# Optimization experiments

Measured on AMD Instinct MI355X. Metric: run time of the kernel, lower is better.

The kernel has to match this reference:

```python
import jax, jax.numpy as jnp
import numpy as np

N, DEG, F, H, OUT = 50000, 16, 128, 128, 64


def _lstm_aggr(neigh, w_ih, w_hh, b_ih, b_hh):
    # neigh: [N, D, F] fixed-degree neighbor features; run LSTM over D steps,
    # return final hidden state [N, H] (PyG SAGEConv 'lstm' aggregation).
    n, d, f = neigh.shape
    h_dim = w_hh.shape[1]

    def step(carry, xt):
        h, c = carry
        gates = xt @ w_ih.T + b_ih + h @ w_hh.T + b_hh  # [N, 4H]
        i, fg, g, o = jnp.split(gates, 4, axis=-1)      # torch gate order i,f,g,o
        i = jax.nn.sigmoid(i)
        fg = jax.nn.sigmoid(fg)
        g = jnp.tanh(g)
        o = jax.nn.sigmoid(o)
        c = fg * c + i * g
        h = o * jnp.tanh(c)
        return (h, c), None

    h0 = jnp.zeros((n, h_dim), neigh.dtype)
    (h, _), _ = jax.lax.scan(step, (h0, h0), jnp.swapaxes(neigh, 0, 1))
    return h


def _sage_lstm(x, src, w_ih, w_hh, b_ih, b_hh, wl, bl, wr):
    # SAGEConv: out = lin_l(lstm_aggr(x[neighbors])) + lin_r(x)
    neigh = x[src]                                   # [N, D, F] gather
    aggr = _lstm_aggr(neigh, w_ih, w_hh, b_ih, b_hh)  # [N, H]
    return aggr @ wl.T + bl + x @ wr.T


def setup_inputs() -> dict:
    key = jax.random.key(0)
    ks = jax.random.split(key, 16)
    x = jax.random.normal(ks[0], (N, F), dtype=jnp.float32)
    # fixed-degree graph: dst = arange(N) each repeated DEG times (sorted, as
    # PyG lstm aggregation requires), src random -> edge_index [2, N*DEG]
    src = jax.random.randint(ks[1], (N * DEG,), 0, N, dtype=jnp.int64)
    dst = jnp.repeat(jnp.arange(N, dtype=jnp.int64), DEG)
    edge_index = jnp.stack([src, dst])
    s = 1.0 / np.sqrt(H)
    def u(k, shape):
        return jax.random.uniform(k, shape, jnp.float32, -s, s)
    params = {
        # layer 1 (input F -> hidden H)
        "w_ih1": u(ks[2], (4 * H, F)), "w_hh1": u(ks[3], (4 * H, H)),
        "b_ih1": u(ks[4], (4 * H,)), "b_hh1": u(ks[5], (4 * H,)),
        "lin_l1_w": u(ks[6], (H, H)), "lin_l1_b": u(ks[6], (H,)),
        "lin_r1_w": u(ks[7], (H, F)),
        # layer 2 (H -> H)
        "w_ih2": u(ks[8], (4 * H, H)), "w_hh2": u(ks[9], (4 * H, H)),
        "b_ih2": u(ks[10], (4 * H,)), "b_hh2": u(ks[11], (4 * H,)),
        "lin_l2_w": u(ks[12], (H, H)), "lin_l2_b": u(ks[12], (H,)),
        "lin_r2_w": u(ks[13], (H, H)),
        # output head
        "lin_w": u(ks[14], (OUT, H)), "lin_b": u(ks[15], (OUT,)),
    }
    return {"x": x, "edge_index": edge_index, **params}


def reference(x, edge_index,
              w_ih1, w_hh1, b_ih1, b_hh1, lin_l1_w, lin_l1_b, lin_r1_w,
              w_ih2, w_hh2, b_ih2, b_hh2, lin_l2_w, lin_l2_b, lin_r2_w,
              lin_w, lin_b):
    n = x.shape[0]
    deg = edge_index.shape[1] // n
    src = edge_index[0].reshape(n, deg)  # fixed-degree neighbor matrix
    h = _sage_lstm(x, src, w_ih1, w_hh1, b_ih1, b_hh1, lin_l1_w, lin_l1_b, lin_r1_w)
    h = jax.nn.relu(h)
    h = _sage_lstm(h, src, w_ih2, w_hh2, b_ih2, b_hh2, lin_l2_w, lin_l2_b, lin_r2_w)
    h = jax.nn.relu(h)
    return h @ lin_w.T + lin_b
```

## Files before the change

### kernel.cpp

```cpp
#include <hip/hip_runtime.h>
#include <stdint.h>

#define NN 50000
#define DEG 16
#define MT 32
#define NBLK ((NN + MT - 1) / MT)
#define LOG2E 1.4426950408889634f

typedef short bf16x8 __attribute__((ext_vector_type(8)));
typedef float f32x4 __attribute__((ext_vector_type(4)));
typedef unsigned short u16;
typedef unsigned int u32;

static __device__ __forceinline__ u16 f2bf(float f) {
  union { float f; u32 u; } v; v.f = f;
  u32 u = v.u + 0x7FFFu + ((v.u >> 16) & 1u);
  return (u16)(u >> 16);
}
static __device__ __forceinline__ float rcp_(float x) {
  return __builtin_amdgcn_rcpf(x);
}
static __device__ __forceinline__ float ex2_(float x) {
  return __builtin_amdgcn_exp2f(x);
}
static __device__ __forceinline__ void gload_lds16(const void* g, void* l) {
  __builtin_amdgcn_global_load_lds(
      (const __attribute__((address_space(1))) void*)g,
      (__attribute__((address_space(3))) void*)l, 16, 0, 0);
}

__global__ void k_prep(const float* __restrict__ x, u16* __restrict__ xb,
                       const float* __restrict__ wih1, const float* __restrict__ whh1, u16* __restrict__ wpk1,
                       const float* __restrict__ wih2, const float* __restrict__ whh2, u16* __restrict__ wpk2,
                       const float* __restrict__ lr1, const float* __restrict__ ll1, u16* __restrict__ epk1,
                       const float* __restrict__ lr2, const float* __restrict__ ll2, u16* __restrict__ epk2,
                       const float* __restrict__ linw, u16* __restrict__ hpk,
                       const float* __restrict__ bi1, const float* __restrict__ bh1, float* __restrict__ bs1,
                       const float* __restrict__ bi2, const float* __restrict__ bh2, float* __restrict__ bs2) {
  int b = blockIdx.x;
  if (b < 128) {
    const float* wih = (b < 64) ? wih1 : wih2;
    const float* whh = (b < 64) ? whh1 : whh2;
    u16* wpk = (b < 64) ? wpk1 : wpk2;
    int t = (b & 63) * 256 + threadIdx.x;
    int lane = t & 63, kt = (t >> 6) & 7, g = (t >> 9) & 3, w = (t >> 11) & 7;
    int col = g * 128 + w * 16 + (lane & 15);
    int k0 = kt * 32 + (lane >> 4) * 8;
    float sc = (g == 2) ? 2.f * LOG2E : LOG2E;
#pragma unroll
    for (int j = 0; j < 8; ++j) {
      int k = k0 + j;
      float v = (k < 128) ? wih[col * 128 + k] : whh[col * 128 + k - 128];
      wpk[t * 8 + j] = f2bf(sc * v);
    }
  } else if (b < 160) {
    const float* lrw = (b < 144) ? lr1 : lr2;
    const float* llw = (b < 144) ? ll1 : ll2;
    u16* epk = (b < 144) ? epk1 : epk2;
    int t = ((b - 128) & 15) * 256 + threadIdx.x;
    int lane = t & 63, kt = (t >> 6) & 7, w = (t >> 9) & 7;
    int col = w * 16 + (lane & 15);
    int k0 = kt * 32 + (lane >> 4) * 8;
#pragma unroll
    for (int j = 0; j < 8; ++j) {
      int k = k0 + j;
      epk[t * 8 + j] = f2bf(k < 128 ? lrw[col * 128 + k] : llw[col * 128 + k - 128]);
    }
  } else if (b < 164) {
    int t = (b - 160) * 256 + threadIdx.x;
    int lane = t & 63, kt = (t >> 6) & 3, w = (t >> 8) & 3;
    int col = w * 16 + (lane & 15);
    int k0 = kt * 32 + (lane >> 4) * 8;
#pragma unroll
    for (int j = 0; j < 8; ++j) hpk[t * 8 + j] = f2bf(linw[col * 128 + k0 + j]);
  } else if (b < 168) {
    int t = (b - 164) * 256 + threadIdx.x;
    if (t < 1024) {
      int i = t & 511;
      float sc = ((i >> 7) == 2) ? 2.f * LOG2E : LOG2E;
      if (t < 512) bs1[i] = sc * (bi1[i] + bh1[i]);
      else bs2[i] = sc * (bi2[i] + bh2[i]);
    }
  } else {
    int i = (b - 168) * 256 + threadIdx.x;
    int stride = (gridDim.x - 168) * 256;
    for (; i < NN * 128 / 4; i += stride) {
      float4 v = ((const float4*)x)[i];
      ushort4 o;
      o.x = f2bf(v.x); o.y = f2bf(v.y); o.z = f2bf(v.z); o.w = f2bf(v.w);
      ((ushort4*)xb)[i] = o;
    }
  }
}


#define GATHER(DCODE, PDST)                                                   \
  do {                                                                        \
    int idx_;                                                                 \
    if ((DCODE) < DEG) idx_ = IDX[grow * DEG + (DCODE)];                      \
    else idx_ = (node0 + grow < NN) ? node0 + grow : NN - 1;                  \
    const char* gsw_ = (const char*)(xin + (size_t)idx_ * 128) +              \
                       ((lr * 16) ^ ((grow & 15) << 4));                      \
    gload_lds16(gsw_, (PDST) + (w * 4) * 128);                                \
  } while (0)

#define GATE_XPART(ACC, PSRC)                                                 \
  do {                                                                        \
    _Pragma("unroll") for (int mt = 0; mt < 2; ++mt)                          \
        _Pragma("unroll") for (int g = 0; g < 4; ++g)                         \
            ACC[mt][g] = (f32x4){gb[g], gb[g], gb[g], gb[g]};                 \
    _Pragma("unroll") for (int kt = 0; kt < 4; ++kt) {                        \
      bf16x8 af0 = *(const bf16x8*)((const char*)(PSRC) + lr * 256 +          \
                                    ((kt * 64 + lh * 16) ^ ((lr & 15) << 4))); \
      bf16x8 af1 = *(const bf16x8*)((const char*)(PSRC) + (16 + lr) * 256 +   \
                                    ((kt * 64 + lh * 16) ^ ((lr & 15) << 4))); \
      _Pragma("unroll") for (int g = 0; g < 4; ++g) {                         \
        ACC[0][g] = __builtin_amdgcn_mfma_f32_16x16x32_bf16(af0, wreg[g][kt], ACC[0][g], 0, 0, 0); \
        ACC[1][g] = __builtin_amdgcn_mfma_f32_16x16x32_bf16(af1, wreg[g][kt], ACC[1][g], 0, 0, 0); \
      }                                                                       \
    }                                                                         \
  } while (0)

#define GATE_HPART(ACC, PSRC)                                                 \
  do {                                                                        \
    _Pragma("unroll") for (int kt = 0; kt < 4; ++kt) {                        \
      bf16x8 af0 = *(const bf16x8*)((const char*)(PSRC) + lr * 256 +          \
                                    ((kt * 64 + lh * 16) ^ ((lr & 15) << 4))); \
      bf16x8 af1 = *(const bf16x8*)((const char*)(PSRC) + (16 + lr) * 256 +   \
                                    ((kt * 64 + lh * 16) ^ ((lr & 15) << 4))); \
      _Pragma("unroll") for (int g = 0; g < 4; ++g) {                         \
        ACC[0][g] = __builtin_amdgcn_mfma_f32_16x16x32_bf16(af0, wreg[g][4 + kt], ACC[0][g], 0, 0, 0); \
        ACC[1][g] = __builtin_amdgcn_mfma_f32_16x16x32_bf16(af1, wreg[g][4 + kt], ACC[1][g], 0, 0, 0); \
      }                                                                       \
    }                                                                         \
  } while (0)

#define GATE_EW(ACC, AHDST)                                                   \
  do {                                                                        \
    _Pragma("unroll") for (int mt = 0; mt < 2; ++mt)                          \
        _Pragma("unroll") for (int r = 0; r < 4; ++r) {                       \
      float iv = rcp_(1.f + ex2_(-ACC[mt][0][r]));                            \
      float fv = rcp_(1.f + ex2_(-ACC[mt][1][r]));                            \
      float gv = 1.f - 2.f * rcp_(1.f + ex2_(ACC[mt][2][r]));                 \
      float ov = rcp_(1.f + ex2_(-ACC[mt][3][r]));                            \
      float cv = fv * c[mt][r] + iv * gv;                                     \
      c[mt][r] = cv;                                                          \
      float th = 1.f - 2.f * rcp_(1.f + ex2_(2.f * LOG2E * cv));              \
      int row = mt * 16 + lh * 4 + r;                                         \
      int jj = 2 * (w * 16 + lr);                                             \
      *(u16*)((char*)(AHDST) + row * 256 + (jj ^ ((row & 15) << 4))) =        \
          f2bf(ov * th);                                                      \
    }                                                                         \
  } while (0)

template <int L2>
__global__ __launch_bounds__(512, 2) void k_layer(
    const u16* __restrict__ xin, const int* __restrict__ src,
    const u16* __restrict__ wpk, const float* __restrict__ bsum,
    const u16* __restrict__ epk, const float* __restrict__ linlb,
    u16* __restrict__ hout, const u16* __restrict__ hpk,
    const float* __restrict__ linb, float* __restrict__ dout) {
  __shared__ __align__(16) u16 AX[3][MT * 128];
  __shared__ __align__(16) u16 AH[2][MT * 128];
  __shared__ int IDX[MT * DEG];

  const int tid = threadIdx.x;
  const int w = tid >> 6, l = tid & 63;
  const int lr = l & 15, lh = l >> 4;
  const int node0 = blockIdx.x * MT;
  const int grow = w * 4 + lh;

  bf16x8 wreg[4][8];
#pragma unroll
  for (int g = 0; g < 4; ++g)
#pragma unroll
    for (int kt = 0; kt < 8; ++kt)
      wreg[g][kt] = *(const bf16x8*)(wpk + (size_t)(((w * 4 + g) * 8 + kt) * 64 + l) * 8);

  IDX[tid] = (node0 + (tid >> 4) < NN) ? src[node0 * DEG + tid] : 0;

  float gb[4];
#pragma unroll
  for (int g = 0; g < 4; ++g) gb[g] = bsum[g * 128 + w * 16 + lr];
  __syncthreads();

  GATHER(0, AX[0]);
  GATHER(1, AX[1]);

  f32x4 c[2];
  c[0] = (f32x4){0.f, 0.f, 0.f, 0.f};
  c[1] = (f32x4){0.f, 0.f, 0.f, 0.f};
  __syncthreads();

  f32x4 accE[2][4], accO[2][4];
  GATE_XPART(accE, AX[0]);

  u16 *p0 = AX[0], *p1 = AX[1], *p2 = AX[2];

#pragma unroll 1
  for (int it = 0; it < 8; ++it) {
    GATHER(2 * it + 2, p2);
    if (it) GATE_HPART(accE, AH[0]);
    GATE_XPART(accO, p1);
    GATE_EW(accE, AH[1]);
    __syncthreads();
    { u16* t_ = p0; p0 = p1; p1 = p2; p2 = t_; }

    if (it < 7) GATHER(2 * it + 3, p2);
    GATE_HPART(accO, AH[1]);
    if (it < 7) GATE_XPART(accE, p1);
    GATE_EW(accO, AH[0]);
    __syncthreads();
    { u16* t_ = p0; p0 = p1; p1 = p2; p2 = t_; }
  }

  float eb = linlb[w * 16 + lr];
  f32x4 eacc[2];
  eacc[0] = (f32x4){eb, eb, eb, eb};
  eacc[1] = (f32x4){eb, eb, eb, eb};
#pragma unroll
  for (int kt = 0; kt < 8; ++kt) {
    const u16* srcb = (kt < 4) ? AX[1] : AH[0];
    int kb = (kt & 3) * 64 + lh * 16;
    bf16x8 af[2];
#pragma unroll
    for (int mt = 0; mt < 2; ++mt) {
      int row = mt * 16 + lr;
      af[mt] = *(const bf16x8*)((const char*)srcb + row * 256 +
                                (kb ^ ((row & 15) << 4)));
    }
    bf16x8 bf = *(const bf16x8*)(epk + (size_t)((w * 8 + kt) * 64 + l) * 8);
#pragma unroll
    for (int mt = 0; mt < 2; ++mt)
      eacc[mt] = __builtin_amdgcn_mfma_f32_16x16x32_bf16(af[mt], bf, eacc[mt], 0, 0, 0);
  }

  if constexpr (!L2) {
#pragma unroll
    for (int mt = 0; mt < 2; ++mt)
#pragma unroll
      for (int r = 0; r < 4; ++r) {
        int node = node0 + mt * 16 + lh * 4 + r;
        if (node < NN) {
          float v = fmaxf(eacc[mt][r], 0.f);
          hout[(size_t)node * 128 + w * 16 + lr] = f2bf(v);
        }
      }
  } else {
#pragma unroll
    for (int mt = 0; mt < 2; ++mt)
#pragma unroll
      for (int r = 0; r < 4; ++r) {
        int row = mt * 16 + lh * 4 + r;
        float v = fmaxf(eacc[mt][r], 0.f);
        int jj = 2 * (w * 16 + lr);
        *(u16*)((char*)AX[0] + row * 256 + (jj ^ ((row & 15) << 4))) = f2bf(v);
      }
    __syncthreads();
    if (w < 4) {
      float hb = linb[w * 16 + lr];
      f32x4 hacc[2];
      hacc[0] = (f32x4){hb, hb, hb, hb};
      hacc[1] = (f32x4){hb, hb, hb, hb};
#pragma unroll
      for (int kt = 0; kt < 4; ++kt) {
        bf16x8 af[2];
#pragma unroll
        for (int mt = 0; mt < 2; ++mt) {
          int row = mt * 16 + lr;
          af[mt] = *(const bf16x8*)((const char*)AX[0] + row * 256 +
                                    ((kt * 64 + lh * 16) ^ ((row & 15) << 4)));
        }
        bf16x8 bf = *(const bf16x8*)(hpk + (size_t)((w * 4 + kt) * 64 + l) * 8);
#pragma unroll
        for (int mt = 0; mt < 2; ++mt)
          hacc[mt] = __builtin_amdgcn_mfma_f32_16x16x32_bf16(af[mt], bf, hacc[mt], 0, 0, 0);
      }
#pragma unroll
      for (int mt = 0; mt < 2; ++mt)
#pragma unroll
        for (int r = 0; r < 4; ++r) {
          int node = node0 + mt * 16 + lh * 4 + r;
          if (node < NN) dout[(size_t)node * 64 + w * 16 + lr] = hacc[mt][r];
        }
    }
  }
}

extern "C" void kernel_launch(void* const* d_in, const int* in_sizes, int n_in,
                              void* d_out, int out_size, void* d_ws, size_t ws_size,
                              hipStream_t stream) {
  const float* x    = (const float*)d_in[0];
  const int*   edge = (const int*)d_in[1];
  const float* wih1 = (const float*)d_in[2];
  const float* whh1 = (const float*)d_in[3];
  const float* bih1 = (const float*)d_in[4];
  const float* bhh1 = (const float*)d_in[5];
  const float* ll1w = (const float*)d_in[6];
  const float* ll1b = (const float*)d_in[7];
  const float* lr1w = (const float*)d_in[8];
  const float* wih2 = (const float*)d_in[9];
  const float* whh2 = (const float*)d_in[10];
  const float* bih2 = (const float*)d_in[11];
  const float* bhh2 = (const float*)d_in[12];
  const float* ll2w = (const float*)d_in[13];
  const float* ll2b = (const float*)d_in[14];
  const float* lr2w = (const float*)d_in[15];
  const float* linw = (const float*)d_in[16];
  const float* linb = (const float*)d_in[17];

  char* ws = (char*)d_ws;
  u16* xb    = (u16*)(ws);
  u16* h1b   = (u16*)(ws + 12800000);
  u16* wpk1  = (u16*)(ws + 25600000);
  u16* wpk2  = (u16*)(ws + 25862144);
  u16* epk1  = (u16*)(ws + 26124288);
  u16* epk2  = (u16*)(ws + 26189824);
  u16* hpk   = (u16*)(ws + 26255360);
  float* bs1 = (float*)(ws + 26271744);
  float* bs2 = (float*)(ws + 26273792);

  k_prep<<<1000, 256, 0, stream>>>(x, xb,
                                   wih1, whh1, wpk1, wih2, whh2, wpk2,
                                   lr1w, ll1w, epk1, lr2w, ll2w, epk2,
                                   linw, hpk,
                                   bih1, bhh1, bs1, bih2, bhh2, bs2);
  k_layer<0><<<NBLK, 512, 0, stream>>>(xb, edge, wpk1, bs1, epk1, ll1b,
                                       h1b, nullptr, nullptr, nullptr);
  k_layer<1><<<NBLK, 512, 0, stream>>>(h1b, edge, wpk2, bs2, epk2, ll2b,
                                       nullptr, hpk, linb, (float*)d_out);
}
```

Before: 591.7 us.

## Load gathered neighbor rows directly into registers instead of LDS staging

Replaces the global_load_lds gather into a triple-buffered shared-memory tile with per-wave direct global loads of each neighbor row into MFMA A-operand registers. The loop is restructured from a two-step even/odd pipeline into a single step loop that loads the next step's x fragments while the current hidden-state part and elementwise gates run. This removes the LDS x buffers and their reads, cutting LDS traffic and footprint. In exchange every wave (all 8) redundantly loads the same 32 rows from global memory, which multiplies gather traffic roughly eightfold (served mostly by cache), adds register pressure, and shortens the prefetch distance.

Measured after the change: 728.5 us. 23.1% more time.

```diff
diff --git a/kernel.cpp b/kernel.cpp
--- a/kernel.cpp
+++ b/kernel.cpp
@@ -22,11 +22,6 @@
 }
 static __device__ __forceinline__ float ex2_(float x) {
   return __builtin_amdgcn_exp2f(x);
-}
-static __device__ __forceinline__ void gload_lds16(const void* g, void* l) {
-  __builtin_amdgcn_global_load_lds(
-      (const __attribute__((address_space(1))) void*)g,
-      (__attribute__((address_space(3))) void*)l, 16, 0, 0);
 }
 
 __global__ void k_prep(const float* __restrict__ x, u16* __restrict__ xb,
@@ -94,55 +89,65 @@
 }
 
 
-#define GATHER(DCODE, PDST)                                                   \
+#define XLOAD(DCODE)                                                          \
   do {                                                                        \
-    int idx_;                                                                 \
-    if ((DCODE) < DEG) idx_ = IDX[grow * DEG + (DCODE)];                      \
-    else idx_ = (node0 + grow < NN) ? node0 + grow : NN - 1;                  \
-    const char* gsw_ = (const char*)(xin + (size_t)idx_ * 128) +              \
-                       ((lr * 16) ^ ((grow & 15) << 4));                      \
-    gload_lds16(gsw_, (PDST) + (w * 4) * 128);                                \
+    int i0_, i1_;                                                             \
+    if ((DCODE) < DEG) {                                                      \
+      i0_ = IDX[lr * DEG + (DCODE)];                                          \
+      i1_ = IDX[(16 + lr) * DEG + (DCODE)];                                   \
+    } else {                                                                  \
+      int n0_ = node0 + lr, n1_ = node0 + 16 + lr;                            \
+      i0_ = (n0_ < NN) ? n0_ : NN - 1;                                        \
+      i1_ = (n1_ < NN) ? n1_ : NN - 1;                                        \
+    }                                                                         \
+    const u16* b0_ = xin + (size_t)i0_ * 128 + lh * 8;                        \
+    const u16* b1_ = xin + (size_t)i1_ * 128 + lh * 8;                        \
+    _Pragma("unroll") for (int kt = 0; kt < 4; ++kt) {                        \
+      xf0[kt] = *(const bf16x8*)(b0_ + kt * 32);                              \
+      xf1[kt] = *(const bf16x8*)(b1_ + kt * 32);                              \
+    }                                                                         \
   } while (0)
 
-#define GATE_XPART(ACC, PSRC)                                                 \
+#define XPART()                                                               \
   do {                                                                        \
-    _Pragma("unroll") for (int mt = 0; mt < 2; ++mt)                          \
-        _Pragma("unroll") for (int g = 0; g < 4; ++g)                         \
-            ACC[mt][g] = (f32x4){gb[g], gb[g], gb[g], gb[g]};                 \
+    _Pragma("unroll") for (int g = 0; g < 4; ++g) {                           \
+      acc0[g] = (f32x4){gb[g], gb[g], gb[g], gb[g]};                          \
+      acc1[g] = (f32x4){gb[g], gb[g], gb[g], gb[g]};                          \
+    }                                                                         \
     _Pragma("unroll") for (int kt = 0; kt < 4; ++kt) {                        \
-      bf16x8 af0 = *(const bf16x8*)((const char*)(PSRC) + lr * 256 +          \
+      _Pragma("unroll") for (int g = 0; g < 4; ++g) {                         \
+        acc0[g] = __builtin_amdgcn_mfma_f32_16x16x32_bf16(xf0[kt], wreg[g][kt], acc0[g], 0, 0, 0); \
+        acc1[g] = __builtin_amdgcn_mfma_f32_16x16x32_bf16(xf1[kt], wreg[g][kt], acc1[g], 0, 0, 0); \
+      }                                                                       \
+    }                                                                         \
+  } while (0)
+
+#define HPART(AHSRC)                                                          \
+  do {                                                                        \
+    _Pragma("unroll") for (int kt = 0; kt < 4; ++kt) {                        \
+      bf16x8 af0 = *(const bf16x8*)((const char*)(AHSRC) + lr * 256 +         \
                                     ((kt * 64 + lh * 16) ^ ((lr & 15) << 4))); \
-      bf16x8 af1 = *(const bf16x8*)((const char*)(PSRC) + (16 + lr) * 256 +   \
+      bf16x8 af1 = *(const bf16x8*)((const char*)(AHSRC) + (16 + lr) * 256 +  \
                                     ((kt * 64 + lh * 16) ^ ((lr & 15) << 4))); \
       _Pragma("unroll") for (int g = 0; g < 4; ++g) {                         \
-        ACC[0][g] = __builtin_amdgcn_mfma_f32_16x16x32_bf16(af0, wreg[g][kt], ACC[0][g], 0, 0, 0); \
-        ACC[1][g] = __builtin_amdgcn_mfma_f32_16x16x32_bf16(af1, wreg[g][kt], ACC[1][g], 0, 0, 0); \
+        acc0[g] = __builtin_amdgcn_mfma_f32_16x16x32_bf16(af0, wreg[g][4 + kt], acc0[g], 0, 0, 0); \
+        acc1[g] = __builtin_amdgcn_mfma_f32_16x16x32_bf16(af1, wreg[g][4 + kt], acc1[g], 0, 0, 0); \
       }                                                                       \
     }                                                                         \
   } while (0)
 
-#define GATE_HPART(ACC, PSRC)                                                 \
-  do {                                                                        \
-    _Pragma("unroll") for (int kt = 0; kt < 4; ++kt) {                        \
-      bf16x8 af0 = *(const bf16x8*)((const char*)(PSRC) + lr * 256 +          \
-                                    ((kt * 64 + lh * 16) ^ ((lr & 15) << 4))); \
-      bf16x8 af1 = *(const bf16x8*)((const char*)(PSRC) + (16 + lr) * 256 +   \
-                                    ((kt * 64 + lh * 16) ^ ((lr & 15) << 4))); \
-      _Pragma("unroll") for (int g = 0; g < 4; ++g) {                         \
-        ACC[0][g] = __builtin_amdgcn_mfma_f32_16x16x32_bf16(af0, wreg[g][4 + kt], ACC[0][g], 0, 0, 0); \
-        ACC[1][g] = __builtin_amdgcn_mfma_f32_16x16x32_bf16(af1, wreg[g][4 + kt], ACC[1][g], 0, 0, 0); \
-      }                                                                       \
-    }                                                                         \
-  } while (0)
-
-#define GATE_EW(ACC, AHDST)                                                   \
+#define GATE_EW(AHDST)                                                        \
   do {                                                                        \
     _Pragma("unroll") for (int mt = 0; mt < 2; ++mt)                          \
         _Pragma("unroll") for (int r = 0; r < 4; ++r) {                       \
-      float iv = rcp_(1.f + ex2_(-ACC[mt][0][r]));                            \
-      float fv = rcp_(1.f + ex2_(-ACC[mt][1][r]));                            \
-      float gv = 1.f - 2.f * rcp_(1.f + ex2_(ACC[mt][2][r]));                 \
-      float ov = rcp_(1.f + ex2_(-ACC[mt][3][r]));                            \
+      float a0 = mt ? acc1[0][r] : acc0[0][r];                                \
+      float a1 = mt ? acc1[1][r] : acc0[1][r];                                \
+      float a2 = mt ? acc1[2][r] : acc0[2][r];                                \
+      float a3 = mt ? acc1[3][r] : acc0[3][r];                                \
+      float iv = rcp_(1.f + ex2_(-a0));                                       \
+      float fv = rcp_(1.f + ex2_(-a1));                                       \
+      float gv = 1.f - 2.f * rcp_(1.f + ex2_(a2));                            \
+      float ov = rcp_(1.f + ex2_(-a3));                                       \
       float cv = fv * c[mt][r] + iv * gv;                                     \
       c[mt][r] = cv;                                                          \
       float th = 1.f - 2.f * rcp_(1.f + ex2_(2.f * LOG2E * cv));              \
@@ -160,7 +165,6 @@
     const u16* __restrict__ epk, const float* __restrict__ linlb,
     u16* __restrict__ hout, const u16* __restrict__ hpk,
     const float* __restrict__ linb, float* __restrict__ dout) {
-  __shared__ __align__(16) u16 AX[3][MT * 128];
   __shared__ __align__(16) u16 AH[2][MT * 128];
   __shared__ int IDX[MT * DEG];
 
@@ -168,7 +172,6 @@
   const int w = tid >> 6, l = tid & 63;
   const int lr = l & 15, lh = l >> 4;
   const int node0 = blockIdx.x * MT;
-  const int grow = w * 4 + lh;
 
   bf16x8 wreg[4][8];
 #pragma unroll
@@ -184,34 +187,24 @@
   for (int g = 0; g < 4; ++g) gb[g] = bsum[g * 128 + w * 16 + lr];
   __syncthreads();
 
-  GATHER(0, AX[0]);
-  GATHER(1, AX[1]);
-
+  bf16x8 xf0[4], xf1[4];
+  f32x4 acc0[4], acc1[4];
   f32x4 c[2];
   c[0] = (f32x4){0.f, 0.f, 0.f, 0.f};
   c[1] = (f32x4){0.f, 0.f, 0.f, 0.f};
-  __syncthreads();
-
-  f32x4 accE[2][4], accO[2][4];
-  GATE_XPART(accE, AX[0]);
-
-  u16 *p0 = AX[0], *p1 = AX[1], *p2 = AX[2];
+
+  XLOAD(0);
+  XPART();
 
 #pragma unroll 1
-  for (int it = 0; it < 8; ++it) {
-    GATHER(2 * it + 2, p2);
-    if (it) GATE_HPART(accE, AH[0]);
-    GATE_XPART(accO, p1);
-    GATE_EW(accE, AH[1]);
+  for (int step = 0; step < DEG; ++step) {
+    const int cb = step & 1, nb = cb ^ 1;
+
+    if (step) HPART(AH[cb]);
+    XLOAD(step + 1);
+    GATE_EW(AH[nb]);
+    if (step < DEG - 1) XPART();
     __syncthreads();
-    { u16* t_ = p0; p0 = p1; p1 = p2; p2 = t_; }
-
-    if (it < 7) GATHER(2 * it + 3, p2);
-    GATE_HPART(accO, AH[1]);
-    if (it < 7) GATE_XPART(accE, p1);
-    GATE_EW(accO, AH[0]);
-    __syncthreads();
-    { u16* t_ = p0; p0 = p1; p1 = p2; p2 = t_; }
   }
 
   float eb = linlb[w * 16 + lr];
@@ -219,17 +212,21 @@
   eacc[0] = (f32x4){eb, eb, eb, eb};
   eacc[1] = (f32x4){eb, eb, eb, eb};
 #pragma unroll
-  for (int kt = 0; kt < 8; ++kt) {
-    const u16* srcb = (kt < 4) ? AX[1] : AH[0];
-    int kb = (kt & 3) * 64 + lh * 16;
+  for (int kt = 0; kt < 4; ++kt) {
+    bf16x8 bf = *(const bf16x8*)(epk + (size_t)((w * 8 + kt) * 64 + l) * 8);
+    eacc[0] = __builtin_amdgcn_mfma_f32_16x16x32_bf16(xf0[kt], bf, eacc[0], 0, 0, 0);
+    eacc[1] = __builtin_amdgcn_mfma_f32_16x16x32_bf16(xf1[kt], bf, eacc[1], 0, 0, 0);
+  }
+#pragma unroll
+  for (int kt = 0; kt < 4; ++kt) {
     bf16x8 af[2];
 #pragma unroll
     for (int mt = 0; mt < 2; ++mt) {
       int row = mt * 16 + lr;
-      af[mt] = *(const bf16x8*)((const char*)srcb + row * 256 +
-                                (kb ^ ((row & 15) << 4)));
-    }
-    bf16x8 bf = *(const bf16x8*)(epk + (size_t)((w * 8 + kt) * 64 + l) * 8);
+      af[mt] = *(const bf16x8*)((const char*)AH[0] + row * 256 +
+                                ((kt * 64 + lh * 16) ^ ((row & 15) << 4)));
+    }
+    bf16x8 bf = *(const bf16x8*)(epk + (size_t)((w * 8 + 4 + kt) * 64 + l) * 8);
 #pragma unroll
     for (int mt = 0; mt < 2; ++mt)
       eacc[mt] = __builtin_amdgcn_mfma_f32_16x16x32_bf16(af[mt], bf, eacc[mt], 0, 0, 0);
@@ -254,7 +251,7 @@
         int row = mt * 16 + lh * 4 + r;
         float v = fmaxf(eacc[mt][r], 0.f);
         int jj = 2 * (w * 16 + lr);
-        *(u16*)((char*)AX[0] + row * 256 + (jj ^ ((row & 15) << 4))) = f2bf(v);
+        *(u16*)((char*)AH[1] + row * 256 + (jj ^ ((row & 15) << 4))) = f2bf(v);
       }
     __syncthreads();
     if (w < 4) {
@@ -268,7 +265,7 @@
 #pragma unroll
         for (int mt = 0; mt < 2; ++mt) {
           int row = mt * 16 + lr;
-          af[mt] = *(const bf16x8*)((const char*)AX[0] + row * 256 +
+          af[mt] = *(const bf16x8*)((const char*)AH[1] + row * 256 +
                                     ((kt * 64 + lh * 16) ^ ((row & 15) << 4)));
         }
         bf16x8 bf = *(const bf16x8*)(hpk + (size_t)((w * 4 + kt) * 64 + l) * 8);
```
